# Kernel optimization log

Hardware: AMD Instinct MI355X
Metric: run time of the kernel (lower is better)

The kernel has to match this reference:

```python
import jax, jax.numpy as jnp
import numpy as np

V_SIZE, E, H = 30000, 256, 128   # vocab, emb_dim, GRU hidden per direction
B, U, T, ND = 32, 32, 128, 64    # dialogues, utterances, max tokens, dialogue-id table size
SCALE = E ** 0.5                  # attention normalise_factor = hid_size**0.5, hid_size = emb_dim


def _gru_dir(x_seq, w_ih, w_hh, b_ih, b_hh):
    """Unidirectional torch-style GRU. x_seq: [N,T,E] -> [N,T,H]."""
    xp = jnp.einsum('nte,ge->ntg', x_seq, w_ih) + b_ih   # precompute input gates [N,T,3H]
    xp = jnp.swapaxes(xp, 0, 1)                          # [T,N,3H]

    def step(h, xpt):
        gh = h @ w_hh.T + b_hh
        r = jax.nn.sigmoid(xpt[:, :H] + gh[:, :H])
        z = jax.nn.sigmoid(xpt[:, H:2 * H] + gh[:, H:2 * H])
        n = jnp.tanh(xpt[:, 2 * H:] + r * gh[:, 2 * H:])
        h_new = (1.0 - z) * n + z * h
        return h_new, h_new

    h0 = jnp.zeros((x_seq.shape[0], H), x_seq.dtype)
    _, out = jax.lax.scan(step, h0, xp)
    return jnp.swapaxes(out, 0, 1)


def _forward(x, d_ids, utt_len, emb_table,
             w_ih_f, w_hh_f, b_ih_f, b_hh_f,
             w_ih_b, w_hh_b, b_ih_b, b_hh_b,
             wq, bq, wk, bk, wv, bv, wo, bo, wl, bl):
    b, u, t = x.shape
    N = b * u
    emb = emb_table[x.reshape(N, t)]                      # [N,T,E]
    lens = jnp.clip(utt_len[d_ids].reshape(N), 1, t)      # valid tokens per utterance
    pos = jnp.arange(t)
    # index map that reverses the valid prefix (padding region clipped, unused)
    rev_idx = jnp.clip(lens[:, None] - 1 - pos[None, :], 0, t - 1)  # [N,T]

    o_f = _gru_dir(emb, w_ih_f, w_hh_f, b_ih_f, b_hh_f)   # causal => correct on valid prefix
    emb_rev = jnp.take_along_axis(emb, rev_idx[:, :, None], axis=1)
    o_b = jnp.take_along_axis(_gru_dir(emb_rev, w_ih_b, w_hh_b, b_ih_b, b_hh_b),
                              rev_idx[:, :, None], axis=1)
    h = jnp.concatenate([o_f, o_b], axis=-1)              # [N,T,E] bi-GRU states

    # self-attention pooling; original takes op[-1], so only the query at the
    # last valid token (lens-1) is needed -- identical math, less compute.
    k = jnp.einsum('nte,he->nth', h, wk) + bk
    v = jnp.einsum('nte,he->nth', h, wv) + bv
    h_last = jnp.take_along_axis(h, (lens - 1)[:, None, None], axis=1)[:, 0]  # [N,E]
    q = h_last @ wq.T + bq
    score = jnp.einsum('nh,nth->nt', q, k) / SCALE
    score = jnp.where(pos[None, :] < lens[:, None], score, -jnp.inf)
    attn = jax.nn.softmax(score, axis=-1)
    ctx = jnp.einsum('nt,nth->nh', attn, v)
    out = (ctx @ wo.T + bo) @ wl.T + bl                   # make_output then final linear
    return out.reshape(b, u, -1)


def setup_inputs() -> dict:
    key = jax.random.key(0)
    ks = jax.random.split(key, 16)

    def p(k, shape):
        return (jax.random.normal(k, shape, jnp.float32) / np.sqrt(shape[-1])).astype(jnp.float32)

    return {
        'x': jax.random.randint(ks[0], (B, U, T), 0, V_SIZE, dtype=jnp.int32),
        'd_ids': jax.random.randint(ks[1], (B,), 0, ND, dtype=jnp.int32),
        'utt_len': jax.random.randint(ks[2], (ND, U), 1, T + 1, dtype=jnp.int32),
        'emb_table': p(ks[3], (V_SIZE, E)),
        'w_ih_f': p(ks[4], (3 * H, E)), 'w_hh_f': p(ks[5], (3 * H, H)),
        'b_ih_f': jnp.zeros(3 * H, jnp.float32), 'b_hh_f': jnp.zeros(3 * H, jnp.float32),
        'w_ih_b': p(ks[6], (3 * H, E)), 'w_hh_b': p(ks[7], (3 * H, H)),
        'b_ih_b': jnp.zeros(3 * H, jnp.float32), 'b_hh_b': jnp.zeros(3 * H, jnp.float32),
        'wq': p(ks[8], (E, E)), 'bq': jnp.zeros(E, jnp.float32),
        'wk': p(ks[9], (E, E)), 'bk': jnp.zeros(E, jnp.float32),
        'wv': p(ks[10], (E, E)), 'bv': jnp.zeros(E, jnp.float32),
        'wo': p(ks[11], (E, E)), 'bo': jnp.zeros(E, jnp.float32),
        'wl': p(ks[12], (E, E)), 'bl': jnp.zeros(E, jnp.float32),
    }


def reference(x, d_ids, utt_len, emb_table,
              w_ih_f, w_hh_f, b_ih_f, b_hh_f,
              w_ih_b, w_hh_b, b_ih_b, b_hh_b,
              wq, bq, wk, bk, wv, bv, wo, bo, wl, bl):
    return _forward(x, d_ids, utt_len, emb_table,
                    w_ih_f, w_hh_f, b_ih_f, b_hh_f,
                    w_ih_b, w_hh_b, b_ih_b, b_hh_b,
                    wq, bq, wk, bk, wv, bv, wo, bo, wl, bl)
```

## Files before the change

### kernel.cpp

```cpp
#include <hip/hip_runtime.h>
#include <hip/hip_bf16.h>
#include <math.h>
#include <stdint.h>

typedef unsigned short u16;
typedef unsigned int   u32;
typedef __attribute__((ext_vector_type(8))) short bf16x8;
typedef __attribute__((ext_vector_type(4))) float f32x4;

#define EDIM 256
#define HDIM 128
#define TLEN 128
#define NUTT 1024
#define UU   32
#define NBU  8

#define WS_FLAG 0
#define WS_LENS 64
#define WS_TAB  4608
#define WS_COPY 8192
#define WS_OF   18874368LL
#define WS_OB   52428800LL

#define MFMA16(a, b, c) __builtin_amdgcn_mfma_f32_16x16x32_bf16((a), (b), (c), 0, 0, 0)
#define SOUT(u, s, j) ((u) * 1096 + (s) * 136 + (j))

__constant__ int G_SZ[18] = {7680000, 98304, 49152, 384, 384, 98304, 49152, 384, 384,
                             65536, 256, 65536, 65536, 256, 65536, 256, 65536, 256};

__device__ __forceinline__ float b2f(u16 b) {
    u32 u = ((u32)b) << 16; float f; __builtin_memcpy(&f, &u, 4); return f;
}
__device__ __forceinline__ u16 f2b(float f) {
    u32 u; __builtin_memcpy(&u, &f, 4);
    u32 r = u + 0x7FFFu + ((u >> 16) & 1u);
    return (u16)(r >> 16);
}
__device__ __forceinline__ u16 f2b_hw(float f) {
    __hip_bfloat16 h = __float2bfloat16(f);
    u16 v; __builtin_memcpy(&v, &h, 2); return v;
}
__device__ __forceinline__ float fsigmoid(float x) { return 1.0f / (1.0f + __expf(-x)); }
__device__ __forceinline__ float ftanh(float x) { return 1.0f - 2.0f / (__expf(2.0f * x) + 1.0f); }

__global__ __launch_bounds__(256)
void k_convert(void* ws,
               const int* __restrict__ d_ids, const int* __restrict__ utt_len,
               const void* a0, const void* a1, const void* a2, const void* a3,
               const void* a4, const void* a5, const void* a6, const void* a7,
               const void* a8, const void* a9, const void* a10, const void* a11,
               const void* a12, const void* a13, const void* a14, const void* a15,
               const void* a16, const void* a17) {
    __shared__ int scnt[4];
    const int tid = threadIdx.x, lane = tid & 63, wid = tid >> 6;
    const u16* p = (const u16*)a0;
    int cnt = 0;
#pragma unroll 8
    for (int i = tid; i < 16384; i += 256)
        cnt += ((p[i] & 0x7F80) == 0x7F80) ? 1 : 0;
#pragma unroll
    for (int o = 32; o > 0; o >>= 1) cnt += __shfl_down(cnt, o);
    if (lane == 0) scnt[wid] = cnt;
    __syncthreads();
    const int flag = (scnt[0] + scnt[1] + scnt[2] + scnt[3] > 0) ? 1 : 0;

    if (blockIdx.x == 0) {
        if (tid == 0) {
            const void* orig[18] = {a0,a1,a2,a3,a4,a5,a6,a7,a8,a9,a10,a11,a12,a13,a14,a15,a16,a17};
            *(int*)((char*)ws + WS_FLAG) = flag;
            const u16** tab = (const u16**)((char*)ws + WS_TAB);
            char* base = (char*)ws + WS_COPY;
            long long cum = 0;
            for (int a = 0; a < 18; ++a) {
                tab[a] = flag ? (const u16*)(base + cum * 2) : (const u16*)orig[a];
                cum += G_SZ[a];
            }
        }
        int* lens = (int*)((char*)ws + WS_LENS);
#pragma unroll 4
        for (int n = tid; n < NUTT; n += 256) {
            int b = n >> 5;
            int u = n & (UU - 1);
            int L = utt_len[d_ids[b] * UU + u];
            lens[n] = min(max(L, 1), TLEN);
        }
    }

    if (flag == 0) return;
    const void* orig[18] = {a0,a1,a2,a3,a4,a5,a6,a7,a8,a9,a10,a11,a12,a13,a14,a15,a16,a17};
    u16* base = (u16*)((char*)ws + WS_COPY);
    const int gtid = blockIdx.x * blockDim.x + tid;
    const int gs   = gridDim.x * blockDim.x;
    long long cum = 0;
    for (int a = 0; a < 18; ++a) {
        const float4* src = (const float4*)orig[a];
        uint2* dst = (uint2*)(base + cum);
        const int n4 = G_SZ[a] >> 2;
        for (int i = gtid; i < n4; i += gs) {
            float4 v = src[i];
            uint2 pk;
            pk.x = (u32)f2b(v.x) | ((u32)f2b(v.y) << 16);
            pk.y = (u32)f2b(v.z) | ((u32)f2b(v.w) << 16);
            dst[i] = pk;
        }
        cum += G_SZ[a];
    }
}

__global__ __launch_bounds__(512)
void k_scan(const int* __restrict__ x, void* ws) {
    const u16* const* tab = (const u16* const*)((char*)ws + WS_TAB);
    const int dir = blockIdx.y;
    const u16* emb  = tab[0];
    const u16* w_ih = tab[1 + dir * 4];
    const u16* w_hh = tab[2 + dir * 4];
    const u16* b_ih = tab[3 + dir * 4];
    const u16* b_hh = tab[4 + dir * 4];
    u16* outp = (u16*)((char*)ws + (dir ? WS_OB : WS_OF));
    const int* lens = (const int*)((char*)ws + WS_LENS);

    const int n0 = blockIdx.x * NBU;
    __shared__ __align__(16) u16 sh_emb[2][NBU][264];
    __shared__ __align__(16) u16 sh_hi[2][NBU * 136];
    __shared__ __align__(16) u16 sh_lo[2][NBU * 136];
    __shared__ __align__(16) u16 sh_out[2][NBU * 1096];
    __shared__ int sh_tok[NBU * TLEN];
    __shared__ int sh_L[NBU];

    const int tid = threadIdx.x, lane = tid & 63, wvi = tid >> 6;
    const int q4 = lane >> 4, mm = lane & 15;
    const int j = wvi * 16 + mm;
    const int u8 = mm & 7;

    for (int i = tid; i < NBU * 136; i += 512) { sh_hi[0][i] = 0; sh_lo[0][i] = 0; }
    for (int i = tid; i < NBU * TLEN; i += 512) {
        const int u = i >> 7, tt = i & 127;
        sh_tok[i] = x[(n0 + u) * TLEN + tt];
    }
    if (tid < NBU) sh_L[tid] = lens[n0 + tid];

    bf16x8 wih[3][8]; bf16x8 whh[3][4];
    float bcr, bcz, bxn, bgn;
#pragma unroll
    for (int n3 = 0; n3 < 3; ++n3) {
        const int g = n3 * HDIM + j;
#pragma unroll
        for (int ks = 0; ks < 8; ++ks)
            wih[n3][ks] = *(const bf16x8*)(w_ih + g * EDIM + ks * 32 + q4 * 8);
#pragma unroll
        for (int ks = 0; ks < 4; ++ks)
            whh[n3][ks] = *(const bf16x8*)(w_hh + g * HDIM + ks * 32 + q4 * 8);
    }
    bcr = b2f(b_ih[j]) + b2f(b_hh[j]);
    bcz = b2f(b_ih[HDIM + j]) + b2f(b_hh[HDIM + j]);
    bxn = b2f(b_ih[2 * HDIM + j]);
    bgn = b2f(b_hh[2 * HDIM + j]);

    const int arr0 = (q4 & 2);
    float hprev[2] = {0.f, 0.f};
    const f32x4 zero4 = {0.f, 0.f, 0.f, 0.f};
    __syncthreads();

    const bool pwave = (wvi < 4);
    const int pf_u = lane & 7;
    const int pf_c = wvi * 8 + (lane >> 3);
    const int pf_L = sh_L[pf_u];

    uint4 pf;
    if (pwave) {
        const int te0 = dir ? (pf_L - 1) : 0;
        const int tok = sh_tok[pf_u * TLEN + te0];
        pf = *(const uint4*)(emb + (size_t)tok * EDIM + pf_c * 8);
        *(uint4*)&sh_emb[0][pf_u][pf_c * 8] = pf;
    }
    __syncthreads();

    for (int t = 0; t < TLEN; ++t) {
        const int cur = t & 1, nxt = cur ^ 1;
        const int obuf = (t >> 3) & 1, slot = t & 7;

        if (pwave && (t + 1 < TLEN)) {
            const int te = dir ? max(pf_L - 2 - t, 0) : (t + 1);
            const int tok = sh_tok[pf_u * TLEN + te];
            pf = *(const uint4*)(emb + (size_t)tok * EDIM + pf_c * 8);
        }

        f32x4 accx[3], accg[3];
        {
            bf16x8 a = *(const bf16x8*)&sh_emb[cur][u8][q4 * 8];
#pragma unroll
            for (int n3 = 0; n3 < 3; ++n3) accx[n3] = MFMA16(a, wih[n3][0], zero4);
        }
#pragma unroll
        for (int ks = 1; ks < 8; ++ks) {
            bf16x8 a = *(const bf16x8*)&sh_emb[cur][u8][ks * 32 + q4 * 8];
#pragma unroll
            for (int n3 = 0; n3 < 3; ++n3) accx[n3] = MFMA16(a, wih[n3][ks], accx[n3]);
        }
        {
            bf16x8 ahi = *(const bf16x8*)(sh_hi[cur] + u8 * 136 + q4 * 8);
            bf16x8 alo = *(const bf16x8*)(sh_lo[cur] + u8 * 136 + q4 * 8);
#pragma unroll
            for (int n3 = 0; n3 < 3; ++n3) {
                accg[n3] = MFMA16(ahi, whh[n3][0], zero4);
                accg[n3] = MFMA16(alo, whh[n3][0], accg[n3]);
            }
        }
#pragma unroll
        for (int ks = 1; ks < 4; ++ks) {
            bf16x8 ahi = *(const bf16x8*)(sh_hi[cur] + u8 * 136 + ks * 32 + q4 * 8);
            bf16x8 alo = *(const bf16x8*)(sh_lo[cur] + u8 * 136 + ks * 32 + q4 * 8);
#pragma unroll
            for (int n3 = 0; n3 < 3; ++n3) {
                accg[n3] = MFMA16(ahi, whh[n3][ks], accg[n3]);
                accg[n3] = MFMA16(alo, whh[n3][ks], accg[n3]);
            }
        }

#pragma unroll
        for (int rr2 = 0; rr2 < 2; ++rr2) {
            const int arr = rr2 + arr0;
            const int u   = (q4 * 4 + arr) & 7;
            const float r  = fsigmoid(accx[0][arr] + accg[0][arr] + bcr);
            const float z  = fsigmoid(accx[1][arr] + accg[1][arr] + bcz);
            const float nn = ftanh((accx[2][arr] + bxn) + r * (accg[2][arr] + bgn));
            const float hn = (1.0f - z) * nn + z * hprev[rr2];
            hprev[rr2] = hn;
            const u16 hb = f2b_hw(hn);
            sh_hi[nxt][u * 136 + j] = hb;
            sh_lo[nxt][u * 136 + j] = f2b_hw(hn - b2f(hb));
            sh_out[obuf][SOUT(u, slot, j)] = hb;
        }

        if (pwave && (t + 1 < TLEN))
            *(uint4*)&sh_emb[nxt][pf_u][pf_c * 8] = pf;

        __syncthreads();

        if (slot == 7) {
            const int rowIdx = tid >> 3;
            const int part   = tid & 7;
            const int fu = rowIdx >> 3, fs = rowIdx & 7;
            const int tt = (t & ~7) + fs;
            const int tout = dir ? (sh_L[fu] - 1 - tt) : tt;
            if (tout >= 0) {
                const u16* srcp = &sh_out[obuf][SOUT(fu, fs, part * 16)];
                uint4 v0 = *(const uint4*)(srcp);
                uint4 v1 = *(const uint4*)(srcp + 8);
                u16* dstp = outp + ((size_t)(n0 + fu) * TLEN + tout) * HDIM + part * 16;
                *(uint4*)(dstp)     = v0;
                *(uint4*)(dstp + 8) = v1;
            }
        }
    }
}

__global__ __launch_bounds__(256)
void k_attn(void* ws, void* outv) {
    const u16* const* tab = (const u16* const*)((char*)ws + WS_TAB);
    const u16* wq = tab[9];  const u16* bq = tab[10];
    const u16* wk = tab[11];
    const u16* wv = tab[12]; const u16* bv = tab[13];
    const u16* wo = tab[14]; const u16* bo = tab[15];
    const u16* wl = tab[16]; const u16* bl = tab[17];
    const int* lens = (const int*)((char*)ws + WS_LENS);
    const int flag = *(const int*)((const char*)ws + WS_FLAG);

    const int n = blockIdx.x;
    const int L = lens[n];
    const u16* hf = (const u16*)((char*)ws + WS_OF) + (size_t)n * TLEN * HDIM;
    const u16* hb = (const u16*)((char*)ws + WS_OB) + (size_t)n * TLEN * HDIM;

    __shared__ float sh_hl[EDIM];
    __shared__ float sh_v1[EDIM];
    __shared__ float sh_uv[EDIM];
    __shared__ float sh_a[4 * EDIM];
    __shared__ float sh_m[4], sh_l[4];

    const int tid = threadIdx.x, lane = tid & 63, wid = tid >> 6;

    sh_hl[tid] = (tid < HDIM) ? b2f(hf[(size_t)(L - 1) * HDIM + tid])
                              : b2f(hb[(size_t)(L - 1) * HDIM + (tid - HDIM)]);
    __syncthreads();

    {
        float s0 = b2f(bq[tid]), s1 = 0.0f;
        const u16* wr = wq + tid * EDIM;
#pragma unroll
        for (int ks = 0; ks < 32; ks += 2) {
            bf16x8 w8 = *(const bf16x8*)(wr + ks * 8);
            bf16x8 w9 = *(const bf16x8*)(wr + ks * 8 + 8);
#pragma unroll
            for (int d = 0; d < 8; ++d) {
                s0 += b2f((u16)w8[d]) * sh_hl[ks * 8 + d];
                s1 += b2f((u16)w9[d]) * sh_hl[ks * 8 + 8 + d];
            }
        }
        sh_v1[tid] = s0 + s1;
    }
    __syncthreads();

    {
        float s0 = 0.0f, s1 = 0.0f;
        for (int i = 0; i < EDIM; i += 2) {
            s0 += b2f(wk[i * EDIM + tid]) * sh_v1[i];
            s1 += b2f(wk[(i + 1) * EDIM + tid]) * sh_v1[i + 1];
        }
        sh_uv[tid] = s0 + s1;
    }
    __syncthreads();

    {
        const int e0 = lane * 4;
        const float u0 = sh_uv[e0], u1 = sh_uv[e0 + 1];
        const float u2 = sh_uv[e0 + 2], u3 = sh_uv[e0 + 3];
        float m = -1e30f, l = 0.0f;
        float a0 = 0.f, a1 = 0.f, a2 = 0.f, a3 = 0.f;
        for (int t = wid; t < L; t += 4) {
            const u16* src = (lane < 32) ? (hf + (size_t)t * HDIM + lane * 4)
                                         : (hb + (size_t)t * HDIM + (lane - 32) * 4);
            uint2 pv = *(const uint2*)src;
            const float h0 = b2f((u16)(pv.x & 0xFFFF));
            const float h1 = b2f((u16)(pv.x >> 16));
            const float h2 = b2f((u16)(pv.y & 0xFFFF));
            const float h3 = b2f((u16)(pv.y >> 16));
            float p = h0 * u0 + h1 * u1 + h2 * u2 + h3 * u3;
#pragma unroll
            for (int o = 32; o > 0; o >>= 1) p += __shfl_xor(p, o);
            const float s = p * 0.0625f;
            const float mn = fmaxf(m, s);
            const float c = __expf(m - mn);
            const float w = __expf(s - mn);
            l = l * c + w;
            a0 = a0 * c + w * h0;
            a1 = a1 * c + w * h1;
            a2 = a2 * c + w * h2;
            a3 = a3 * c + w * h3;
            m = mn;
        }
        sh_a[wid * EDIM + e0]     = a0;
        sh_a[wid * EDIM + e0 + 1] = a1;
        sh_a[wid * EDIM + e0 + 2] = a2;
        sh_a[wid * EDIM + e0 + 3] = a3;
        if (lane == 0) { sh_m[wid] = m; sh_l[wid] = l; }
    }
    __syncthreads();

    {
        const float m0 = sh_m[0], m1 = sh_m[1], m2 = sh_m[2], m3 = sh_m[3];
        const float M = fmaxf(fmaxf(m0, m1), fmaxf(m2, m3));
        const float c0 = __expf(m0 - M), c1 = __expf(m1 - M);
        const float c2 = __expf(m2 - M), c3 = __expf(m3 - M);
        const float den = c0 * sh_l[0] + c1 * sh_l[1] + c2 * sh_l[2] + c3 * sh_l[3];
        const float num = c0 * sh_a[tid] + c1 * sh_a[EDIM + tid] +
                          c2 * sh_a[2 * EDIM + tid] + c3 * sh_a[3 * EDIM + tid];
        sh_hl[tid] = num / den;
    }
    __syncthreads();

    {
        float s0 = b2f(bv[tid]), s1 = 0.0f;
        const u16* wr = wv + tid * EDIM;
#pragma unroll
        for (int ks = 0; ks < 32; ks += 2) {
            bf16x8 w8 = *(const bf16x8*)(wr + ks * 8);
            bf16x8 w9 = *(const bf16x8*)(wr + ks * 8 + 8);
#pragma unroll
            for (int d = 0; d < 8; ++d) {
                s0 += b2f((u16)w8[d]) * sh_hl[ks * 8 + d];
                s1 += b2f((u16)w9[d]) * sh_hl[ks * 8 + 8 + d];
            }
        }
        sh_uv[tid] = s0 + s1;
    }
    __syncthreads();

    {
        float s0 = b2f(bo[tid]), s1 = 0.0f;
        const u16* wr = wo + tid * EDIM;
#pragma unroll
        for (int ks = 0; ks < 32; ks += 2) {
            bf16x8 w8 = *(const bf16x8*)(wr + ks * 8);
            bf16x8 w9 = *(const bf16x8*)(wr + ks * 8 + 8);
#pragma unroll
            for (int d = 0; d < 8; ++d) {
                s0 += b2f((u16)w8[d]) * sh_uv[ks * 8 + d];
                s1 += b2f((u16)w9[d]) * sh_uv[ks * 8 + 8 + d];
            }
        }
        sh_v1[tid] = s0 + s1;
    }
    __syncthreads();

    {
        float s0 = b2f(bl[tid]), s1 = 0.0f;
        const u16* wr = wl + tid * EDIM;
#pragma unroll
        for (int ks = 0; ks < 32; ks += 2) {
            bf16x8 w8 = *(const bf16x8*)(wr + ks * 8);
            bf16x8 w9 = *(const bf16x8*)(wr + ks * 8 + 8);
#pragma unroll
            for (int d = 0; d < 8; ++d) {
                s0 += b2f((u16)w8[d]) * sh_v1[ks * 8 + d];
                s1 += b2f((u16)w9[d]) * sh_v1[ks * 8 + 8 + d];
            }
        }
        const float s = s0 + s1;
        const size_t oidx = (size_t)n * EDIM + tid;
        if (flag) ((float*)outv)[oidx] = s;
        else      ((u16*)outv)[oidx]   = f2b(s);
    }
}

extern "C" void kernel_launch(void* const* d_in, const int* in_sizes, int n_in,
                              void* d_out, int out_size, void* d_ws, size_t ws_size,
                              hipStream_t stream) {
    const int* x       = (const int*)d_in[0];
    const int* d_ids   = (const int*)d_in[1];
    const int* utt_len = (const int*)d_in[2];
    const void* f_arr[18] = {
        d_in[3],
        d_in[4], d_in[5], d_in[6], d_in[7],
        d_in[8], d_in[9], d_in[10], d_in[11],
        d_in[12], d_in[13],
        d_in[14],
        d_in[16], d_in[17],
        d_in[18], d_in[19],
        d_in[20], d_in[21]
    };

    k_convert<<<512, 256, 0, stream>>>(d_ws, d_ids, utt_len,
        f_arr[0], f_arr[1], f_arr[2], f_arr[3], f_arr[4], f_arr[5], f_arr[6], f_arr[7],
        f_arr[8], f_arr[9], f_arr[10], f_arr[11], f_arr[12], f_arr[13], f_arr[14],
        f_arr[15], f_arr[16], f_arr[17]);

    k_scan<<<dim3(NUTT / NBU, 2), 512, 0, stream>>>(x, d_ws);

    k_attn<<<NUTT, 256, 0, stream>>>(d_ws, d_out);
}
```

Before: 402.9 us.

## Pipeline GRU input projection one step ahead and stop scan at group max length

```diff
diff --git a/kernel.cpp b/kernel.cpp
--- a/kernel.cpp
+++ b/kernel.cpp
@@ -124,7 +124,7 @@
     __shared__ __align__(16) u16 sh_hi[2][NBU * 136];
     __shared__ __align__(16) u16 sh_lo[2][NBU * 136];
     __shared__ __align__(16) u16 sh_out[2][NBU * 1096];
-    __shared__ int sh_tok[NBU * TLEN];
+    __shared__ int sh_tok[NBU * 132];
     __shared__ int sh_L[NBU];
 
     const int tid = threadIdx.x, lane = tid & 63, wvi = tid >> 6;
@@ -135,7 +135,7 @@
     for (int i = tid; i < NBU * 136; i += 512) { sh_hi[0][i] = 0; sh_lo[0][i] = 0; }
     for (int i = tid; i < NBU * TLEN; i += 512) {
         const int u = i >> 7, tt = i & 127;
-        sh_tok[i] = x[(n0 + u) * TLEN + tt];
+        sh_tok[u * 132 + tt] = x[(n0 + u) * TLEN + tt];
     }
     if (tid < NBU) sh_L[tid] = lens[n0 + tid];
 
@@ -161,6 +161,11 @@
     const f32x4 zero4 = {0.f, 0.f, 0.f, 0.f};
     __syncthreads();
 
+    int Lm = sh_L[0];
+#pragma unroll
+    for (int u = 1; u < NBU; ++u) Lm = max(Lm, sh_L[u]);
+    const int tmax = (Lm + 7) & ~7;
+
     const bool pwave = (wvi < 4);
     const int pf_u = lane & 7;
     const int pf_c = wvi * 8 + (lane >> 3);
@@ -169,34 +174,42 @@
     uint4 pf;
     if (pwave) {
         const int te0 = dir ? (pf_L - 1) : 0;
-        const int tok = sh_tok[pf_u * TLEN + te0];
-        pf = *(const uint4*)(emb + (size_t)tok * EDIM + pf_c * 8);
-        *(uint4*)&sh_emb[0][pf_u][pf_c * 8] = pf;
-    }
-    __syncthreads();
-
-    for (int t = 0; t < TLEN; ++t) {
+        const int tok0 = sh_tok[pf_u * 132 + te0];
+        uint4 v0 = *(const uint4*)(emb + (size_t)tok0 * EDIM + pf_c * 8);
+        *(uint4*)&sh_emb[0][pf_u][pf_c * 8] = v0;
+        const int te1 = dir ? max(pf_L - 2, 0) : 1;
+        const int tok1 = sh_tok[pf_u * 132 + te1];
+        uint4 v1 = *(const uint4*)(emb + (size_t)tok1 * EDIM + pf_c * 8);
+        *(uint4*)&sh_emb[1][pf_u][pf_c * 8] = v1;
+    }
+    __syncthreads();
+
+    f32x4 accx_cur[3];
+    {
+        bf16x8 a = *(const bf16x8*)&sh_emb[0][u8][q4 * 8];
+#pragma unroll
+        for (int n3 = 0; n3 < 3; ++n3) accx_cur[n3] = MFMA16(a, wih[n3][0], zero4);
+#pragma unroll
+        for (int ks = 1; ks < 8; ++ks) {
+            bf16x8 a2 = *(const bf16x8*)&sh_emb[0][u8][ks * 32 + q4 * 8];
+#pragma unroll
+            for (int n3 = 0; n3 < 3; ++n3) accx_cur[n3] = MFMA16(a2, wih[n3][ks], accx_cur[n3]);
+        }
+    }
+    __syncthreads();
+
+    for (int t = 0; t < tmax; ++t) {
         const int cur = t & 1, nxt = cur ^ 1;
         const int obuf = (t >> 3) & 1, slot = t & 7;
-
-        if (pwave && (t + 1 < TLEN)) {
-            const int te = dir ? max(pf_L - 2 - t, 0) : (t + 1);
-            const int tok = sh_tok[pf_u * TLEN + te];
+        const bool more = (t + 2 < tmax);
+
+        if (pwave && more) {
+            const int te = dir ? max(pf_L - 3 - t, 0) : (t + 2);
+            const int tok = sh_tok[pf_u * 132 + te];
             pf = *(const uint4*)(emb + (size_t)tok * EDIM + pf_c * 8);
         }
 
-        f32x4 accx[3], accg[3];
-        {
-            bf16x8 a = *(const bf16x8*)&sh_emb[cur][u8][q4 * 8];
-#pragma unroll
-            for (int n3 = 0; n3 < 3; ++n3) accx[n3] = MFMA16(a, wih[n3][0], zero4);
-        }
-#pragma unroll
-        for (int ks = 1; ks < 8; ++ks) {
-            bf16x8 a = *(const bf16x8*)&sh_emb[cur][u8][ks * 32 + q4 * 8];
-#pragma unroll
-            for (int n3 = 0; n3 < 3; ++n3) accx[n3] = MFMA16(a, wih[n3][ks], accx[n3]);
-        }
+        f32x4 accg[3];
         {
             bf16x8 ahi = *(const bf16x8*)(sh_hi[cur] + u8 * 136 + q4 * 8);
             bf16x8 alo = *(const bf16x8*)(sh_lo[cur] + u8 * 136 + q4 * 8);
@@ -217,13 +230,26 @@
             }
         }
 
+        f32x4 accx_nxt[3];
+        if (t + 1 < tmax) {
+            bf16x8 a = *(const bf16x8*)&sh_emb[nxt][u8][q4 * 8];
+#pragma unroll
+            for (int n3 = 0; n3 < 3; ++n3) accx_nxt[n3] = MFMA16(a, wih[n3][0], zero4);
+#pragma unroll
+            for (int ks = 1; ks < 8; ++ks) {
+                bf16x8 a2 = *(const bf16x8*)&sh_emb[nxt][u8][ks * 32 + q4 * 8];
+#pragma unroll
+                for (int n3 = 0; n3 < 3; ++n3) accx_nxt[n3] = MFMA16(a2, wih[n3][ks], accx_nxt[n3]);
+            }
+        }
+
 #pragma unroll
         for (int rr2 = 0; rr2 < 2; ++rr2) {
             const int arr = rr2 + arr0;
             const int u   = (q4 * 4 + arr) & 7;
-            const float r  = fsigmoid(accx[0][arr] + accg[0][arr] + bcr);
-            const float z  = fsigmoid(accx[1][arr] + accg[1][arr] + bcz);
-            const float nn = ftanh((accx[2][arr] + bxn) + r * (accg[2][arr] + bgn));
+            const float r  = fsigmoid(accx_cur[0][arr] + accg[0][arr] + bcr);
+            const float z  = fsigmoid(accx_cur[1][arr] + accg[1][arr] + bcz);
+            const float nn = ftanh((accx_cur[2][arr] + bxn) + r * (accg[2][arr] + bgn));
             const float hn = (1.0f - z) * nn + z * hprev[rr2];
             hprev[rr2] = hn;
             const u16 hb = f2b_hw(hn);
@@ -232,8 +258,13 @@
             sh_out[obuf][SOUT(u, slot, j)] = hb;
         }
 
-        if (pwave && (t + 1 < TLEN))
-            *(uint4*)&sh_emb[nxt][pf_u][pf_c * 8] = pf;
+        if (pwave && more)
+            *(uint4*)&sh_emb[cur][pf_u][pf_c * 8] = pf;
+
+        if (t + 1 < tmax) {
+#pragma unroll
+            for (int n3 = 0; n3 < 3; ++n3) accx_cur[n3] = accx_nxt[n3];
+        }
 
         __syncthreads();
 
```

Result: no change. 410.3 us (+1.8%).
